# Kernel tuning notes

Hardware: AMD Instinct MI355X
Metric: run time of the kernel (lower is better)

## Reference

```python
import jax, jax.numpy as jnp
import numpy as np

DIM = 300


def setup_inputs() -> dict:
    key = jax.random.key(0)
    k1, k2, k3, k4, k5 = jax.random.split(key, 5)
    options, batch = 5, 100000
    answer_vector = jax.random.normal(k1, (options, batch, 2 * DIM), dtype=jnp.float32)
    h = DIM // 4  # 75
    # torch nn.Linear default init: U(-1/sqrt(fan_in), 1/sqrt(fan_in)); values irrelevant for correctness test
    s1 = 1.0 / np.sqrt(2 * DIM)
    s2 = 1.0 / np.sqrt(h)
    W1 = jax.random.uniform(k2, (h, 2 * DIM), jnp.float32, -s1, s1)
    b1 = jax.random.uniform(k3, (h,), jnp.float32, -s1, s1)
    W2 = jax.random.uniform(k4, (1, h), jnp.float32, -s2, s2)
    b2 = jax.random.uniform(k5, (1,), jnp.float32, -s2, s2)
    return {"answer_vector": answer_vector, "W1": W1, "b1": b1, "W2": W2, "b2": b2}


def reference(answer_vector, W1, b1, W2, b2) -> jnp.ndarray:
    # answer_vector: [options, batch, 600]
    h = jax.nn.relu(jnp.einsum('obd,hd->obh', answer_vector, W1) + b1)  # [O,B,75]
    score = jnp.einsum('obh,kh->obk', h, W2)[..., 0] + b2[0]            # [O,B]
    return score.T  # [batch, options]
```

## Files before the change

kernel.cpp:

```cpp
#include <hip/hip_runtime.h>
#include <hip/hip_bf16.h>

#define NOPT    5
#define NBATCH  100000
#define MTOT    (NOPT * NBATCH)
#define KDIM    600
#define BM      64
#define NKS     19
#define NT      5

typedef __bf16 bf16x8 __attribute__((ext_vector_type(8)));
typedef float  f32x4  __attribute__((ext_vector_type(4)));

__device__ __forceinline__ int kstart(int s) { return (s < 18) ? (s << 5) : 568; }

__global__ void prep_w1(const float* __restrict__ W1, __bf16* __restrict__ img) {
    const int s  = blockIdx.x / NT;
    const int t  = blockIdx.x % NT;
    const int l  = threadIdx.x;
    const int kg = l >> 4;
    const int n  = t * 16 + (l & 15);
    const int ks = kstart(s);
    bf16x8 v;
#pragma unroll
    for (int j = 0; j < 8; ++j) {
        const int k = ks + kg * 8 + j;
        float f = 0.0f;
        if (n < 75 && !(s == 18 && kg == 0)) f = W1[n * KDIM + k];
        v[j] = (__bf16)f;
    }
    *(bf16x8*)(img + ((size_t)blockIdx.x * 64 + l) * 8) = v;
}

__global__ void __launch_bounds__(256) ans_sel_kernel(
    const float* __restrict__ A,
    const float* __restrict__ b1,
    const float* __restrict__ W2,
    const float* __restrict__ b2,
    const __bf16* __restrict__ img,
    float* __restrict__ out)
{
    __shared__ float  As[2][2048];
    __shared__ __bf16 Bs[2][2560];

    const int tid  = threadIdx.x;
    const int w    = tid >> 6;
    const int l    = tid & 63;
    const int kg   = l >> 4;
    const int ln16 = l & 15;
    const int row0 = blockIdx.x * BM;

    f32x4 acc[NT];
#pragma unroll
    for (int t = 0; t < NT; ++t) acc[t] = (f32x4){0.f, 0.f, 0.f, 0.f};

    const int a_r0 = w * 16 + (l >> 3);
    const int a_r1 = a_r0 + 8;
    const int pch  = l & 7;

    auto stage = [&](int buf, int s) {
        const int k0 = kstart(s);
        {
            const int c   = pch ^ (a_r0 & 7);
            int gr = row0 + a_r0; if (gr >= MTOT) gr = MTOT - 1;
            __builtin_amdgcn_global_load_lds(
                (const __attribute__((address_space(1))) void*)(A + (size_t)gr * KDIM + k0 + c * 4),
                (__attribute__((address_space(3))) void*)(&As[buf][(w * 2) * 256]),
                16, 0, 0);
        }
        {
            const int c   = pch ^ (a_r1 & 7);
            int gr = row0 + a_r1; if (gr >= MTOT) gr = MTOT - 1;
            __builtin_amdgcn_global_load_lds(
                (const __attribute__((address_space(1))) void*)(A + (size_t)gr * KDIM + k0 + c * 4),
                (__attribute__((address_space(3))) void*)(&As[buf][(w * 2 + 1) * 256]),
                16, 0, 0);
        }
        for (int i = w; i < NT; i += 4) {
            __builtin_amdgcn_global_load_lds(
                (const __attribute__((address_space(1))) void*)(img + (size_t)s * 2560 + i * 512 + l * 8),
                (__attribute__((address_space(3))) void*)(&Bs[buf][i * 512]),
                16, 0, 0);
        }
    };

    auto compute = [&](int buf) {
        const int r  = w * 16 + ln16;
        const f32x4* af = (const f32x4*)As[buf];
        const int c0 = kg * 2;
        f32x4 fa0 = af[r * 8 + ((c0    ) ^ (r & 7))];
        f32x4 fa1 = af[r * 8 + ((c0 + 1) ^ (r & 7))];
        bf16x8 a;
        a[0] = (__bf16)fa0[0]; a[1] = (__bf16)fa0[1];
        a[2] = (__bf16)fa0[2]; a[3] = (__bf16)fa0[3];
        a[4] = (__bf16)fa1[0]; a[5] = (__bf16)fa1[1];
        a[6] = (__bf16)fa1[2]; a[7] = (__bf16)fa1[3];
#pragma unroll
        for (int t = 0; t < NT; ++t) {
            bf16x8 b = *(const bf16x8*)(&Bs[buf][t * 512 + l * 8]);
            acc[t] = __builtin_amdgcn_mfma_f32_16x16x32_bf16(a, b, acc[t], 0, 0, 0);
        }
    };

    stage(0, 0);
    __syncthreads();
    int cur = 0;
    for (int s = 0; s < NKS - 1; ++s) {
        stage(cur ^ 1, s + 1);
        compute(cur);
        __syncthreads();
        cur ^= 1;
    }
    compute(cur);

    float sq[4] = {0.f, 0.f, 0.f, 0.f};
#pragma unroll
    for (int t = 0; t < NT; ++t) {
        const int n = t * 16 + ln16;
        const float b1v = (n < 75) ? b1[n] : 0.f;
        const float w2v = (n < 75) ? W2[n] : 0.f;
#pragma unroll
        for (int q = 0; q < 4; ++q) {
            float h = acc[t][q] + b1v;
            h = h > 0.f ? h : 0.f;
            sq[q] += h * w2v;
        }
    }
#pragma unroll
    for (int m = 1; m < 16; m <<= 1) {
#pragma unroll
        for (int q = 0; q < 4; ++q) sq[q] += __shfl_xor(sq[q], m, 64);
    }
    if (ln16 == 0) {
        const float bb = b2[0];
#pragma unroll
        for (int q = 0; q < 4; ++q) {
            const int R = row0 + w * 16 + kg * 4 + q;
            if (R < MTOT) {
                const int o = R / NBATCH;
                const int b = R % NBATCH;
                out[(size_t)b * NOPT + o] = sq[q] + bb;
            }
        }
    }
}

extern "C" void kernel_launch(void* const* d_in, const int* in_sizes, int n_in,
                              void* d_out, int out_size, void* d_ws, size_t ws_size,
                              hipStream_t stream) {
    const float* A  = (const float*)d_in[0];
    const float* W1 = (const float*)d_in[1];
    const float* b1 = (const float*)d_in[2];
    const float* W2 = (const float*)d_in[3];
    const float* b2 = (const float*)d_in[4];
    float* out = (float*)d_out;
    __bf16* img = (__bf16*)d_ws;

    prep_w1<<<NKS * NT, 64, 0, stream>>>(W1, img);

    const int grid = (MTOT + BM - 1) / BM;
    ans_sel_kernel<<<grid, 256, 0, stream>>>(A, b1, W2, b2, img, out);
}
```

Before: 267.5 us.

## Replace LDS double-buffered staging with direct register loads and prefetch

Drops the shared-memory staging of A and W1 tiles (global_load_lds plus __syncthreads) and has each lane load its A fragment and B fragments straight from global memory into registers. The next k-step is prefetched into registers while the current one feeds the MFMAs. This removes the barriers and LDS traffic. In exchange each lane issues two 16-byte loads per row, each touching only part of a 128-byte line, so coalescing gets worse, and more registers are used.

```diff
diff --git a/kernel.cpp b/kernel.cpp
--- a/kernel.cpp
+++ b/kernel.cpp
@@ -5,7 +5,6 @@
 #define NBATCH  100000
 #define MTOT    (NOPT * NBATCH)
 #define KDIM    600
-#define BM      64
 #define NKS     19
 #define NT      5
 
@@ -40,78 +39,61 @@
     const __bf16* __restrict__ img,
     float* __restrict__ out)
 {
-    __shared__ float  As[2][2048];
-    __shared__ __bf16 Bs[2][2560];
-
     const int tid  = threadIdx.x;
     const int w    = tid >> 6;
     const int l    = tid & 63;
     const int kg   = l >> 4;
     const int ln16 = l & 15;
-    const int row0 = blockIdx.x * BM;
+    const int rowbase = blockIdx.x * 64 + w * 16;
+
+    int gr = rowbase + ln16; if (gr >= MTOT) gr = MTOT - 1;
+    const float*  ap = A + (size_t)gr * KDIM + kg * 8;
+    const __bf16* bp = img + (size_t)l * 8;
 
     f32x4 acc[NT];
 #pragma unroll
     for (int t = 0; t < NT; ++t) acc[t] = (f32x4){0.f, 0.f, 0.f, 0.f};
 
-    const int a_r0 = w * 16 + (l >> 3);
-    const int a_r1 = a_r0 + 8;
-    const int pch  = l & 7;
-
-    auto stage = [&](int buf, int s) {
-        const int k0 = kstart(s);
-        {
-            const int c   = pch ^ (a_r0 & 7);
-            int gr = row0 + a_r0; if (gr >= MTOT) gr = MTOT - 1;
-            __builtin_amdgcn_global_load_lds(
-                (const __attribute__((address_space(1))) void*)(A + (size_t)gr * KDIM + k0 + c * 4),
-                (__attribute__((address_space(3))) void*)(&As[buf][(w * 2) * 256]),
-                16, 0, 0);
-        }
-        {
-            const int c   = pch ^ (a_r1 & 7);
-            int gr = row0 + a_r1; if (gr >= MTOT) gr = MTOT - 1;
-            __builtin_amdgcn_global_load_lds(
-                (const __attribute__((address_space(1))) void*)(A + (size_t)gr * KDIM + k0 + c * 4),
-                (__attribute__((address_space(3))) void*)(&As[buf][(w * 2 + 1) * 256]),
-                16, 0, 0);
-        }
-        for (int i = w; i < NT; i += 4) {
-            __builtin_amdgcn_global_load_lds(
-                (const __attribute__((address_space(1))) void*)(img + (size_t)s * 2560 + i * 512 + l * 8),
-                (__attribute__((address_space(3))) void*)(&Bs[buf][i * 512]),
-                16, 0, 0);
-        }
+    auto LDA = [&](int s, f32x4& x0, f32x4& x1) {
+        const float* p = ap + kstart(s);
+        x0 = *(const f32x4*)(p);
+        x1 = *(const f32x4*)(p + 4);
+    };
+    auto LDB = [&](int s, bf16x8& b0v, bf16x8& b1v, bf16x8& b2v, bf16x8& b3v, bf16x8& b4v) {
+        const __bf16* p = bp + (size_t)s * (NT * 512);
+        b0v = *(const bf16x8*)(p);
+        b1v = *(const bf16x8*)(p + 512);
+        b2v = *(const bf16x8*)(p + 1024);
+        b3v = *(const bf16x8*)(p + 1536);
+        b4v = *(const bf16x8*)(p + 2048);
+    };
+    auto CMP = [&](f32x4 x0, f32x4 x1, bf16x8 b0v, bf16x8 b1v, bf16x8 b2v, bf16x8 b3v, bf16x8 b4v) {
+        bf16x8 a;
+        a[0] = (__bf16)x0[0]; a[1] = (__bf16)x0[1];
+        a[2] = (__bf16)x0[2]; a[3] = (__bf16)x0[3];
+        a[4] = (__bf16)x1[0]; a[5] = (__bf16)x1[1];
+        a[6] = (__bf16)x1[2]; a[7] = (__bf16)x1[3];
+        acc[0] = __builtin_amdgcn_mfma_f32_16x16x32_bf16(a, b0v, acc[0], 0, 0, 0);
+        acc[1] = __builtin_amdgcn_mfma_f32_16x16x32_bf16(a, b1v, acc[1], 0, 0, 0);
+        acc[2] = __builtin_amdgcn_mfma_f32_16x16x32_bf16(a, b2v, acc[2], 0, 0, 0);
+        acc[3] = __builtin_amdgcn_mfma_f32_16x16x32_bf16(a, b3v, acc[3], 0, 0, 0);
+        acc[4] = __builtin_amdgcn_mfma_f32_16x16x32_bf16(a, b4v, acc[4], 0, 0, 0);
     };
 
-    auto compute = [&](int buf) {
-        const int r  = w * 16 + ln16;
-        const f32x4* af = (const f32x4*)As[buf];
-        const int c0 = kg * 2;
-        f32x4 fa0 = af[r * 8 + ((c0    ) ^ (r & 7))];
-        f32x4 fa1 = af[r * 8 + ((c0 + 1) ^ (r & 7))];
-        bf16x8 a;
-        a[0] = (__bf16)fa0[0]; a[1] = (__bf16)fa0[1];
-        a[2] = (__bf16)fa0[2]; a[3] = (__bf16)fa0[3];
-        a[4] = (__bf16)fa1[0]; a[5] = (__bf16)fa1[1];
-        a[6] = (__bf16)fa1[2]; a[7] = (__bf16)fa1[3];
-#pragma unroll
-        for (int t = 0; t < NT; ++t) {
-            bf16x8 b = *(const bf16x8*)(&Bs[buf][t * 512 + l * 8]);
-            acc[t] = __builtin_amdgcn_mfma_f32_16x16x32_bf16(a, b, acc[t], 0, 0, 0);
-        }
-    };
+    f32x4 ca0, ca1, na0, na1;
+    bf16x8 cb0, cb1, cb2, cb3, cb4, nb0, nb1, nb2, nb3, nb4;
 
-    stage(0, 0);
-    __syncthreads();
-    int cur = 0;
+    LDA(0, ca0, ca1);
+    LDB(0, cb0, cb1, cb2, cb3, cb4);
+#pragma unroll 2
     for (int s = 0; s < NKS - 1; ++s) {
-        stage(cur ^ 1, s + 1);
-        compute(cur);
-        __syncthreads();
-        cur ^= 1;
+        LDA(s + 1, na0, na1);
+        LDB(s + 1, nb0, nb1, nb2, nb3, nb4);
+        CMP(ca0, ca1, cb0, cb1, cb2, cb3, cb4);
+        ca0 = na0; ca1 = na1;
+        cb0 = nb0; cb1 = nb1; cb2 = nb2; cb3 = nb3; cb4 = nb4;
     }
-    compute(cur);
+    CMP(ca0, ca1, cb0, cb1, cb2, cb3, cb4);
 
     float sq[4] = {0.f, 0.f, 0.f, 0.f};
 #pragma unroll
@@ -135,7 +117,7 @@
         const float bb = b2[0];
 #pragma unroll
         for (int q = 0; q < 4; ++q) {
-            const int R = row0 + w * 16 + kg * 4 + q;
+            const int R = rowbase + kg * 4 + q;
             if (R < MTOT) {
                 const int o = R / NBATCH;
                 const int b = R % NBATCH;
@@ -158,6 +140,6 @@
 
     prep_w1<<<NKS * NT, 64, 0, stream>>>(W1, img);
 
-    const int grid = (MTOT + BM - 1) / BM;
+    const int grid = (MTOT + 63) / 64;
     ans_sel_kernel<<<grid, 256, 0, stream>>>(A, b1, W2, b2, img, out);
 }
```

Measured after the change: 349.6 us. 30.7% more time.

## Stage 64-wide K tiles per barrier and read W1 fragments directly from global

Applied to the files above, without the earlier changes.

Each double-buffer stage of the A tile now covers 64 columns of K instead of 32, which halves the number of __syncthreads barriers, with a 16-way XOR swizzle and precomputed row pointers. The bf16 W1 image is no longer staged through LDS. Each wave reads its B fragments straight from global memory, relying on caches since the image is small and shared by all blocks. A launch-bounds occupancy hint is also added. The risk is extra global and L2 latency on the B loads inside the MFMA loop.

```diff
diff --git a/kernel.cpp b/kernel.cpp
--- a/kernel.cpp
+++ b/kernel.cpp
@@ -5,8 +5,6 @@
 #define NBATCH  100000
 #define MTOT    (NOPT * NBATCH)
 #define KDIM    600
-#define BM      64
-#define NKS     19
 #define NT      5
 
 typedef __bf16 bf16x8 __attribute__((ext_vector_type(8)));
@@ -32,7 +30,7 @@
     *(bf16x8*)(img + ((size_t)blockIdx.x * 64 + l) * 8) = v;
 }
 
-__global__ void __launch_bounds__(256) ans_sel_kernel(
+__global__ void __launch_bounds__(256, 4) ans_sel_kernel(
     const float* __restrict__ A,
     const float* __restrict__ b1,
     const float* __restrict__ W2,
@@ -40,78 +38,120 @@
     const __bf16* __restrict__ img,
     float* __restrict__ out)
 {
-    __shared__ float  As[2][2048];
-    __shared__ __bf16 Bs[2][2560];
+    __shared__ f32x4 As[2][4][256];
 
     const int tid  = threadIdx.x;
     const int w    = tid >> 6;
     const int l    = tid & 63;
     const int kg   = l >> 4;
     const int ln16 = l & 15;
-    const int row0 = blockIdx.x * BM;
+    const int row0 = blockIdx.x * 64;
+
+    const int r16 = l >> 4;
+    const int c16 = l & 15;
+    const float* ap0; const float* ap1; const float* ap2; const float* ap3;
+    {
+        int r, gr;
+        r = w * 16 + 0 * 4 + r16; gr = row0 + r; if (gr >= MTOT) gr = MTOT - 1;
+        ap0 = A + (size_t)gr * KDIM + ((c16 ^ (r & 15)) << 2);
+        r = w * 16 + 1 * 4 + r16; gr = row0 + r; if (gr >= MTOT) gr = MTOT - 1;
+        ap1 = A + (size_t)gr * KDIM + ((c16 ^ (r & 15)) << 2);
+        r = w * 16 + 2 * 4 + r16; gr = row0 + r; if (gr >= MTOT) gr = MTOT - 1;
+        ap2 = A + (size_t)gr * KDIM + ((c16 ^ (r & 15)) << 2);
+        r = w * 16 + 3 * 4 + r16; gr = row0 + r; if (gr >= MTOT) gr = MTOT - 1;
+        ap3 = A + (size_t)gr * KDIM + ((c16 ^ (r & 15)) << 2);
+    }
+    const int r8 = l >> 3;
+    const int c8 = l & 7;
+    const float* at0; const float* at1;
+    {
+        int r, gr;
+        r = w * 16 + 0 * 8 + r8; gr = row0 + r; if (gr >= MTOT) gr = MTOT - 1;
+        at0 = A + (size_t)gr * KDIM + 568 + ((c8 ^ (r & 7)) << 2);
+        r = w * 16 + 1 * 8 + r8; gr = row0 + r; if (gr >= MTOT) gr = MTOT - 1;
+        at1 = A + (size_t)gr * KDIM + 568 + ((c8 ^ (r & 7)) << 2);
+    }
+
+    auto stage64 = [&](int buf, int S) {
+        const int k0 = S * 64;
+        __builtin_amdgcn_global_load_lds(
+            (const __attribute__((address_space(1))) void*)(ap0 + k0),
+            (__attribute__((address_space(3))) void*)(&As[buf][w][0]),   16, 0, 0);
+        __builtin_amdgcn_global_load_lds(
+            (const __attribute__((address_space(1))) void*)(ap1 + k0),
+            (__attribute__((address_space(3))) void*)(&As[buf][w][64]),  16, 0, 0);
+        __builtin_amdgcn_global_load_lds(
+            (const __attribute__((address_space(1))) void*)(ap2 + k0),
+            (__attribute__((address_space(3))) void*)(&As[buf][w][128]), 16, 0, 0);
+        __builtin_amdgcn_global_load_lds(
+            (const __attribute__((address_space(1))) void*)(ap3 + k0),
+            (__attribute__((address_space(3))) void*)(&As[buf][w][192]), 16, 0, 0);
+    };
+    auto stageTail = [&](int buf) {
+        __builtin_amdgcn_global_load_lds(
+            (const __attribute__((address_space(1))) void*)(at0),
+            (__attribute__((address_space(3))) void*)(&As[buf][w][0]),   16, 0, 0);
+        __builtin_amdgcn_global_load_lds(
+            (const __attribute__((address_space(1))) void*)(at1),
+            (__attribute__((address_space(3))) void*)(&As[buf][w][64]),  16, 0, 0);
+    };
 
     f32x4 acc[NT];
 #pragma unroll
     for (int t = 0; t < NT; ++t) acc[t] = (f32x4){0.f, 0.f, 0.f, 0.f};
 
-    const int a_r0 = w * 16 + (l >> 3);
-    const int a_r1 = a_r0 + 8;
-    const int pch  = l & 7;
-
-    auto stage = [&](int buf, int s) {
-        const int k0 = kstart(s);
-        {
-            const int c   = pch ^ (a_r0 & 7);
-            int gr = row0 + a_r0; if (gr >= MTOT) gr = MTOT - 1;
-            __builtin_amdgcn_global_load_lds(
-                (const __attribute__((address_space(1))) void*)(A + (size_t)gr * KDIM + k0 + c * 4),
-                (__attribute__((address_space(3))) void*)(&As[buf][(w * 2) * 256]),
-                16, 0, 0);
-        }
-        {
-            const int c   = pch ^ (a_r1 & 7);
-            int gr = row0 + a_r1; if (gr >= MTOT) gr = MTOT - 1;
-            __builtin_amdgcn_global_load_lds(
-                (const __attribute__((address_space(1))) void*)(A + (size_t)gr * KDIM + k0 + c * 4),
-                (__attribute__((address_space(3))) void*)(&As[buf][(w * 2 + 1) * 256]),
-                16, 0, 0);
-        }
-        for (int i = w; i < NT; i += 4) {
-            __builtin_amdgcn_global_load_lds(
-                (const __attribute__((address_space(1))) void*)(img + (size_t)s * 2560 + i * 512 + l * 8),
-                (__attribute__((address_space(3))) void*)(&Bs[buf][i * 512]),
-                16, 0, 0);
-        }
-    };
-
-    auto compute = [&](int buf) {
-        const int r  = w * 16 + ln16;
-        const f32x4* af = (const f32x4*)As[buf];
-        const int c0 = kg * 2;
-        f32x4 fa0 = af[r * 8 + ((c0    ) ^ (r & 7))];
-        f32x4 fa1 = af[r * 8 + ((c0 + 1) ^ (r & 7))];
+    const __bf16* bp = img + (size_t)l * 8;
+
+    auto sub64 = [&](int buf, int s32, int o) {
+        const f32x4* base = &As[buf][w][ln16 * 16];
+        f32x4 fa0 = base[(o    ) ^ ln16];
+        f32x4 fa1 = base[(o + 1) ^ ln16];
         bf16x8 a;
         a[0] = (__bf16)fa0[0]; a[1] = (__bf16)fa0[1];
         a[2] = (__bf16)fa0[2]; a[3] = (__bf16)fa0[3];
         a[4] = (__bf16)fa1[0]; a[5] = (__bf16)fa1[1];
         a[6] = (__bf16)fa1[2]; a[7] = (__bf16)fa1[3];
+        const __bf16* p = bp + (size_t)s32 * (NT * 512);
 #pragma unroll
         for (int t = 0; t < NT; ++t) {
-            bf16x8 b = *(const bf16x8*)(&Bs[buf][t * 512 + l * 8]);
+            bf16x8 b = *(const bf16x8*)(p + t * 512);
             acc[t] = __builtin_amdgcn_mfma_f32_16x16x32_bf16(a, b, acc[t], 0, 0, 0);
         }
     };
-
-    stage(0, 0);
+    auto compute64 = [&](int buf, int S) {
+        sub64(buf, 2 * S,     kg * 2);
+        sub64(buf, 2 * S + 1, 8 + kg * 2);
+    };
+    auto computeTail = [&](int buf) {
+        const f32x4* base = &As[buf][w][ln16 * 8];
+        const int o = kg * 2;
+        f32x4 fa0 = base[(o    ) ^ (ln16 & 7)];
+        f32x4 fa1 = base[(o + 1) ^ (ln16 & 7)];
+        bf16x8 a;
+        a[0] = (__bf16)fa0[0]; a[1] = (__bf16)fa0[1];
+        a[2] = (__bf16)fa0[2]; a[3] = (__bf16)fa0[3];
+        a[4] = (__bf16)fa1[0]; a[5] = (__bf16)fa1[1];
+        a[6] = (__bf16)fa1[2]; a[7] = (__bf16)fa1[3];
+        const __bf16* p = bp + (size_t)18 * (NT * 512);
+#pragma unroll
+        for (int t = 0; t < NT; ++t) {
+            bf16x8 b = *(const bf16x8*)(p + t * 512);
+            acc[t] = __builtin_amdgcn_mfma_f32_16x16x32_bf16(a, b, acc[t], 0, 0, 0);
+        }
+    };
+
+    stage64(0, 0);
     __syncthreads();
-    int cur = 0;
-    for (int s = 0; s < NKS - 1; ++s) {
-        stage(cur ^ 1, s + 1);
-        compute(cur);
+    int buf = 0;
+#pragma unroll 1
+    for (int S = 0; S < 9; ++S) {
+        if (S < 8) stage64(buf ^ 1, S + 1);
+        else       stageTail(buf ^ 1);
+        compute64(buf, S);
         __syncthreads();
-        cur ^= 1;
-    }
-    compute(cur);
+        buf ^= 1;
+    }
+    computeTail(buf);
 
     float sq[4] = {0.f, 0.f, 0.f, 0.f};
 #pragma unroll
@@ -156,8 +196,8 @@
     float* out = (float*)d_out;
     __bf16* img = (__bf16*)d_ws;
 
-    prep_w1<<<NKS * NT, 64, 0, stream>>>(W1, img);
-
-    const int grid = (MTOT + BM - 1) / BM;
+    prep_w1<<<19 * NT, 64, 0, stream>>>(W1, img);
+
+    const int grid = (MTOT + 63) / 64;
     ans_sel_kernel<<<grid, 256, 0, stream>>>(A, b1, W2, b2, img, out);
 }
```

Result: slower. 295.5 us (+10.5%).
